# Optimization experiments

Measured on AMD Instinct MI355X. Metric: run time of the kernel, lower is better.

The kernel has to match this reference:

```python
import jax, jax.numpy as jnp
import numpy as np

B, D_IN, D_OUT, N_SUBNET, G = 16384, 512, 512, 8, 2


def setup_inputs() -> dict:
    key = jax.random.key(0)
    k_x, k_g, k_w = jax.random.split(key, 3)
    x = jax.random.normal(k_x, (B, D_IN), dtype=jnp.float32)
    groups = jax.random.randint(k_g, (B, G), 0, N_SUBNET, dtype=jnp.int32)
    # per-expert Dense params (the 'subnets')
    W = jax.random.normal(k_w, (N_SUBNET, D_IN, D_OUT), dtype=jnp.float32) * (1.0 / np.sqrt(D_IN))
    b = jnp.zeros((N_SUBNET, D_OUT), dtype=jnp.float32)
    return {"x": x, "groups": groups, "W": W, "b": b}


def reference(x, groups, W, b):
    """SubnetGate: one-hot gated dispatch to per-group subnets + combine.

    Faithful math: gates = one_hot(groups[:, group_col], n_subnet);
    out = sum_e gates[:, e] * subnet_e(x). Since gates are one-hot the
    combine selects exactly one expert output per row (gate weight 1.0).
    """
    group_col = 0
    n_subnet = W.shape[0]
    idx_group = groups[:, group_col]                     # [B]
    gates = jax.nn.one_hot(idx_group, n_subnet, dtype=x.dtype)  # [B, E]
    # run every expert on the full batch (dense reference for the
    # gather-compute-scatter kernel), then gate-combine
    expert_out = jnp.einsum("bi,eio->beo", x, W) + b[None, :, :]  # [B, E, O]
    out = jnp.einsum("be,beo->bo", gates, expert_out)             # [B, O]
    return out
```

## Files before the change

### kernel.cpp

```cpp
#include <hip/hip_runtime.h>
#include <hip/hip_bf16.h>


#define NROWS   16384
#define KDIM    512
#define NDIM    512
#define NEXP    8
#define BM      64
#define BN      128
#define BK      64
#define NT_PER  4
#define KT_PER  8
#define TILE_ELEMS (BN * BK)
#define WS_ROWLIST_OFF 4096
#define WS_WT_OFF      (4096 + NEXP * NROWS * 4)

typedef __bf16        bf16x8 __attribute__((ext_vector_type(8)));
typedef float         f32x4  __attribute__((ext_vector_type(4)));
typedef unsigned int  u32x4  __attribute__((ext_vector_type(4)));

__device__ __forceinline__ unsigned int f2bf_u(float f) {
    unsigned int u = __builtin_bit_cast(unsigned int, f);
    return (u + 0x7FFFu + ((u >> 16) & 1u)) >> 16;
}

__device__ __forceinline__ void gl_lds16(const void* g, void* l) {
    __builtin_amdgcn_global_load_lds(
        (const __attribute__((address_space(1))) unsigned int*)g,
        (__attribute__((address_space(3))) unsigned int*)l, 16, 0, 0);
}

__device__ __forceinline__ bf16x8 pack_bf8(f32x4 lo, f32x4 hi) {
    u32x4 w;
    w.x = f2bf_u(lo.x) | (f2bf_u(lo.y) << 16);
    w.y = f2bf_u(lo.z) | (f2bf_u(lo.w) << 16);
    w.z = f2bf_u(hi.x) | (f2bf_u(hi.y) << 16);
    w.w = f2bf_u(hi.z) | (f2bf_u(hi.w) << 16);
    return __builtin_bit_cast(bf16x8, w);
}

__global__ void prep_kernel(const float* __restrict__ W,
                            const int* __restrict__ groups,
                            int* __restrict__ gcnt,
                            int* __restrict__ rowlist,
                            unsigned short* __restrict__ Wtile) {
    __shared__ __align__(16) unsigned short tl4[32 * 64];
    __shared__ int lcnt[NEXP];
    __shared__ int lbase[NEXP];
    const int bid = blockIdx.x;
    const int tid = threadIdx.x;

    if (bid < 1024) {
        const int tile = bid >> 2;
        const int qq   = bid & 3;
        const int e  = tile >> 5;
        const int nt = (tile >> 3) & 3;
        const int kt = tile & 7;
        const float* Wb = W + (size_t)e * (KDIM * NDIM);

        const int n   = qq * 32 + (tid & 31);
        const int g   = tid >> 5;
        const int col = nt * BN + n;
        unsigned int p[4];
        #pragma unroll
        for (int jj = 0; jj < 4; ++jj) {
            int k0 = kt * BK + g * 8 + jj * 2;
            unsigned int lo = f2bf_u(Wb[(size_t)k0 * NDIM + col]);
            unsigned int hi = f2bf_u(Wb[(size_t)(k0 + 1) * NDIM + col]);
            p[jj] = lo | (hi << 16);
        }
        *(u32x4*)&tl4[(n & 31) * 64 + (g ^ (n & 7)) * 8] = *(const u32x4*)p;
        __syncthreads();
        unsigned short* dst = Wtile + (size_t)tile * TILE_ELEMS
                                    + ((size_t)qq * 256 + tid) * 8;
        *(u32x4*)dst = *(const u32x4*)&tl4[tid * 8];
    } else {
        const int base = (bid - 1024) * 256;
        if (tid < NEXP) lcnt[tid] = 0;
        __syncthreads();
        int r = base + tid;
        int e = groups[r * 2] & 7;
        int pos = atomicAdd(&lcnt[e], 1);
        __syncthreads();
        if (tid < NEXP) lbase[tid] = atomicAdd(&gcnt[tid], lcnt[tid]);
        __syncthreads();
        rowlist[e * NROWS + lbase[e] + pos] = r;
    }
}

__global__ __launch_bounds__(256, 4)
void gemm_kernel(const float* __restrict__ x,
                 const int* __restrict__ counts,
                 const int* __restrict__ rowlist,
                 const unsigned short* __restrict__ Wtile,
                 const float* __restrict__ bias,
                 float* __restrict__ out) {
    __shared__ __align__(16) unsigned short Bsm[2][TILE_ELEMS];

    const int bid = blockIdx.x;
    const int e   = bid & 7;
    const int j   = bid >> 3;
    const int nt  = j & 3;
    const int mt  = j >> 2;
    const int cnt = counts[e];
    const int rb  = mt * BM;
    if (rb >= cnt) return;
    int m_valid = cnt - rb;
    if (m_valid > BM) m_valid = BM;
    const int* rl = rowlist + e * NROWS + rb;

    const int tid = threadIdx.x;
    const int w   = tid >> 6;
    const int ln  = tid & 63;
    const int q   = ln >> 4;
    const int l15 = ln & 15;

    const int am = w * 16 + l15;
    const float* aptr = x + (size_t)rl[(am < m_valid) ? am : 0] * KDIM + q * 8;

    const unsigned short* wt =
        Wtile + (size_t)((e * NT_PER + nt) * KT_PER) * TILE_ELEMS;

    f32x4 a0, a1, a2, a3;
    f32x4 acc[8];
    #pragma unroll
    for (int ni = 0; ni < 8; ++ni) acc[ni] = (f32x4){0.f, 0.f, 0.f, 0.f};

    #pragma unroll
    for (int i = 0; i < 4; ++i) {
        int off = (i * 256 + tid) * 8;
        gl_lds16(wt + off, &Bsm[0][off]);
    }
    a0 = *(const f32x4*)aptr;
    a1 = *(const f32x4*)(aptr + 4);
    a2 = *(const f32x4*)(aptr + 32);
    a3 = *(const f32x4*)(aptr + 36);

    for (int kt = 0; kt < KT_PER; ++kt) {
        __syncthreads();
        if (kt < KT_PER - 1) {
            const unsigned short* src = wt + (size_t)(kt + 1) * TILE_ELEMS;
            unsigned short* dstl = Bsm[(kt + 1) & 1];
            #pragma unroll
            for (int i = 0; i < 4; ++i) {
                int off = (i * 256 + tid) * 8;
                gl_lds16(src + off, dstl + off);
            }
        }
        bf16x8 af0 = pack_bf8(a0, a1);
        bf16x8 af1 = pack_bf8(a2, a3);
        if (kt < KT_PER - 1) {
            const float* s = aptr + (kt + 1) * BK;
            a0 = *(const f32x4*)s;
            a1 = *(const f32x4*)(s + 4);
            a2 = *(const f32x4*)(s + 32);
            a3 = *(const f32x4*)(s + 36);
        }
        const unsigned short* bcur = Bsm[kt & 1];
        #pragma unroll
        for (int ni = 0; ni < 8; ++ni) {
            int n = ni * 16 + l15;
            bf16x8 b0 = *(const bf16x8*)&bcur[n * 64 + (q ^ (n & 7)) * 8];
            acc[ni] = __builtin_amdgcn_mfma_f32_16x16x32_bf16(af0, b0, acc[ni], 0, 0, 0);
        }
        #pragma unroll
        for (int ni = 0; ni < 8; ++ni) {
            int n = ni * 16 + l15;
            bf16x8 b1 = *(const bf16x8*)&bcur[n * 64 + ((4 + q) ^ (n & 7)) * 8];
            acc[ni] = __builtin_amdgcn_mfma_f32_16x16x32_bf16(af1, b1, acc[ni], 0, 0, 0);
        }
    }

    int grow[4];
    #pragma unroll
    for (int r = 0; r < 4; ++r) {
        int mloc = w * 16 + q * 4 + r;
        grow[r] = (mloc < m_valid) ? rl[mloc] : -1;
    }
    const int ncol0 = nt * BN;
    #pragma unroll
    for (int ni = 0; ni < 8; ++ni) {
        int col = ncol0 + ni * 16 + l15;
        float bv = bias[e * NDIM + col];
        #pragma unroll
        for (int r = 0; r < 4; ++r)
            if (grow[r] >= 0)
                __builtin_nontemporal_store(acc[ni][r] + bv,
                                            &out[(size_t)grow[r] * NDIM + col]);
    }
}

extern "C" void kernel_launch(void* const* d_in, const int* in_sizes, int n_in,
                              void* d_out, int out_size, void* d_ws, size_t ws_size,
                              hipStream_t stream) {
    const float* x      = (const float*)d_in[0];
    const int*   groups = (const int*)d_in[1];
    const float* W      = (const float*)d_in[2];
    const float* b      = (const float*)d_in[3];
    float*       out    = (float*)d_out;

    char* ws = (char*)d_ws;
    int*            counts  = (int*)ws;
    int*            rowlist = (int*)(ws + WS_ROWLIST_OFF);
    unsigned short* Wtile   = (unsigned short*)(ws + WS_WT_OFF);

    hipMemsetAsync(counts, 0, NEXP * sizeof(int), stream);
    prep_kernel<<<1088, 256, 0, stream>>>(W, groups, counts, rowlist, Wtile);
    gemm_kernel<<<8192, 256, 0, stream>>>(x, counts, rowlist, Wtile, b, out);
}
```

Baseline: 128.2 us.

## Double M tile, pre-convert x to bf16, 4-stage B pipeline, ballot-based rowlist

The GEMM M tile grows from 64 to 128 rows, so each wave computes two 16-row fragments and each B tile loaded into LDS is reused twice as much. The prep kernel now also converts x to bf16 in workspace when there is room, halving A-load bytes and removing per-k-step packing in the GEMM. B staging moves to a 4-buffer pipeline with explicit waitcnt, barriers and setprio. Rowlist construction switches from global atomics to a deterministic ballot/prefix scheme with one block per expert, and the memset is dropped. In exchange there is higher register and LDS use (launch bounds 2), an extra pass over x, and a serial 8-block rowlist step.

```diff
diff --git a/kernel.cpp b/kernel.cpp
--- a/kernel.cpp
+++ b/kernel.cpp
@@ -6,7 +6,7 @@
 #define KDIM    512
 #define NDIM    512
 #define NEXP    8
-#define BM      64
+#define BM      128
 #define BN      128
 #define BK      64
 #define NT_PER  4
@@ -14,6 +14,8 @@
 #define TILE_ELEMS (BN * BK)
 #define WS_ROWLIST_OFF 4096
 #define WS_WT_OFF      (4096 + NEXP * NROWS * 4)
+#define WS_XG_OFF      (WS_WT_OFF + (size_t)NEXP * NT_PER * KT_PER * TILE_ELEMS * 2)
+#define WS_NEEDED      (WS_XG_OFF + (size_t)NROWS * KDIM * 2)
 
 typedef __bf16        bf16x8 __attribute__((ext_vector_type(8)));
 typedef float         f32x4  __attribute__((ext_vector_type(4)));
@@ -40,19 +42,58 @@
 }
 
 __global__ void prep_kernel(const float* __restrict__ W,
+                            const float* __restrict__ x,
                             const int* __restrict__ groups,
-                            int* __restrict__ gcnt,
+                            int* __restrict__ counts,
                             int* __restrict__ rowlist,
-                            unsigned short* __restrict__ Wtile) {
-    __shared__ __align__(16) unsigned short tl4[32 * 64];
-    __shared__ int lcnt[NEXP];
-    __shared__ int lbase[NEXP];
+                            unsigned short* __restrict__ Wtile,
+                            unsigned short* __restrict__ xg) {
     const int bid = blockIdx.x;
     const int tid = threadIdx.x;
 
-    if (bid < 1024) {
-        const int tile = bid >> 2;
-        const int qq   = bid & 3;
+    if (bid < 8) {
+        __shared__ int wcnt_s[4];
+        __shared__ int woff_s[4];
+        __shared__ int runb;
+        const int e  = bid;
+        const int w  = tid >> 6;
+        const int ln = tid & 63;
+        const unsigned long long below = (ln == 63) ? ~0ull >> 1
+                                                    : (1ull << ln) - 1;
+        int* dst = rowlist + e * NROWS;
+        if (tid == 0) runb = 0;
+        __syncthreads();
+        for (int it = 0; it < NROWS / 1024; ++it) {
+            int rbase = it * 1024 + tid * 4;
+            u32x4 ga = *(const u32x4*)&groups[rbase * 2];
+            u32x4 gb = *(const u32x4*)&groups[rbase * 2 + 4];
+            bool h0 = ((int)ga.x == e), h1 = ((int)ga.z == e);
+            bool h2 = ((int)gb.x == e), h3 = ((int)gb.z == e);
+            unsigned long long m0 = __ballot(h0), m1 = __ballot(h1);
+            unsigned long long m2 = __ballot(h2), m3 = __ballot(h3);
+            int c0 = __popcll(m0), c1 = __popcll(m1), c2 = __popcll(m2);
+            if (ln == 0) wcnt_s[w] = c0 + c1 + c2 + __popcll(m3);
+            __syncthreads();
+            if (tid == 0) {
+                int s = runb;
+                #pragma unroll
+                for (int i = 0; i < 4; ++i) { woff_s[i] = s; s += wcnt_s[i]; }
+                runb = s;
+            }
+            __syncthreads();
+            int base = woff_s[w];
+            if (h0) dst[base + __popcll(m0 & below)] = rbase;
+            if (h1) dst[base + c0 + __popcll(m1 & below)] = rbase + 1;
+            if (h2) dst[base + c0 + c1 + __popcll(m2 & below)] = rbase + 2;
+            if (h3) dst[base + c0 + c1 + c2 + __popcll(m3 & below)] = rbase + 3;
+            __syncthreads();
+        }
+        if (tid == 0) counts[e] = runb;
+    } else if (bid < 1032) {
+        __shared__ __align__(16) unsigned short tl4[32 * 64];
+        const int tb   = bid - 8;
+        const int tile = tb >> 2;
+        const int qq   = tb & 3;
         const int e  = tile >> 5;
         const int nt = (tile >> 3) & 3;
         const int kt = tile & 7;
@@ -75,27 +116,87 @@
                                     + ((size_t)qq * 256 + tid) * 8;
         *(u32x4*)dst = *(const u32x4*)&tl4[tid * 8];
     } else {
-        const int base = (bid - 1024) * 256;
-        if (tid < NEXP) lcnt[tid] = 0;
-        __syncthreads();
-        int r = base + tid;
-        int e = groups[r * 2] & 7;
-        int pos = atomicAdd(&lcnt[e], 1);
-        __syncthreads();
-        if (tid < NEXP) lbase[tid] = atomicAdd(&gcnt[tid], lcnt[tid]);
-        __syncthreads();
-        rowlist[e * NROWS + lbase[e] + pos] = r;
-    }
-}
-
-__global__ __launch_bounds__(256, 4)
+        const size_t base = ((size_t)(bid - 1032) * 256 + tid) * 16;
+        f32x4 v0 = *(const f32x4*)&x[base];
+        f32x4 v1 = *(const f32x4*)&x[base + 4];
+        f32x4 v2 = *(const f32x4*)&x[base + 8];
+        f32x4 v3 = *(const f32x4*)&x[base + 12];
+        *(bf16x8*)&xg[base]     = pack_bf8(v0, v1);
+        *(bf16x8*)&xg[base + 8] = pack_bf8(v2, v3);
+    }
+}
+
+
+#define STAGE_B(KT, BUF)                                                     \
+    {                                                                        \
+        const unsigned short* _src = wt + (size_t)(KT) * TILE_ELEMS;         \
+        _Pragma("unroll")                                                    \
+        for (int _i = 0; _i < 4; ++_i) {                                     \
+            int _off = (_i * 256 + tid) * 8;                                 \
+            gl_lds16(_src + _off, &Bsm[BUF][_off]);                          \
+        }                                                                    \
+    }
+
+#define LOAD_A_XG(KT, AR)                                                    \
+    {                                                                        \
+        const unsigned short* _p0 = arow0 + (KT) * BK + q * 8;               \
+        const unsigned short* _p1 = arow1 + (KT) * BK + q * 8;               \
+        AR[0][0] = *(const bf16x8*)_p0;                                      \
+        AR[0][1] = *(const bf16x8*)(_p0 + 32);                               \
+        AR[1][0] = *(const bf16x8*)_p1;                                      \
+        AR[1][1] = *(const bf16x8*)(_p1 + 32);                               \
+    }
+
+#define LOAD_A_F32(KT, AR)                                                   \
+    {                                                                        \
+        const float* _p0 = afrow0 + (KT) * BK + q * 8;                       \
+        const float* _p1 = afrow1 + (KT) * BK + q * 8;                       \
+        AR[0][0] = pack_bf8(*(const f32x4*)_p0, *(const f32x4*)(_p0 + 4));   \
+        AR[0][1] = pack_bf8(*(const f32x4*)(_p0 + 32),                       \
+                            *(const f32x4*)(_p0 + 36));                      \
+        AR[1][0] = pack_bf8(*(const f32x4*)_p1, *(const f32x4*)(_p1 + 4));   \
+        AR[1][1] = pack_bf8(*(const f32x4*)(_p1 + 32),                       \
+                            *(const f32x4*)(_p1 + 36));                      \
+    }
+
+#define COMPUTE(BUF, AR)                                                     \
+    {                                                                        \
+        _Pragma("unroll")                                                    \
+        for (int _h = 0; _h < 2; ++_h) {                                     \
+            _Pragma("unroll")                                                \
+            for (int _ni = 0; _ni < 8; ++_ni) {                              \
+                int _n = _ni * 16 + l15;                                     \
+                bf16x8 _bf = *(const bf16x8*)&Bsm[BUF][_n * 64 +             \
+                             ((_h * 4 + q) ^ (_n & 7)) * 8];                 \
+                acc[0][_ni] = __builtin_amdgcn_mfma_f32_16x16x32_bf16(       \
+                    AR[0][_h], _bf, acc[0][_ni], 0, 0, 0);                   \
+                acc[1][_ni] = __builtin_amdgcn_mfma_f32_16x16x32_bf16(       \
+                    AR[1][_h], _bf, acc[1][_ni], 0, 0, 0);                   \
+            }                                                                \
+        }                                                                    \
+    }
+
+#define KSTEP(KT, ACUR, ANXT, LOADA)                                         \
+    {                                                                        \
+        asm volatile("s_waitcnt vmcnt(12)" ::: "memory");                    \
+        __builtin_amdgcn_s_barrier();                                        \
+        __builtin_amdgcn_sched_barrier(0);                                   \
+        if ((KT) + 3 < KT_PER) STAGE_B((KT) + 3, ((KT) + 3) & 3)             \
+        if ((KT) + 1 < KT_PER) LOADA((KT) + 1, ANXT)                         \
+        __builtin_amdgcn_s_setprio(1);                                       \
+        COMPUTE((KT) & 3, ACUR)                                              \
+        __builtin_amdgcn_s_setprio(0);                                       \
+    }
+
+__global__ __launch_bounds__(256, 2)
 void gemm_kernel(const float* __restrict__ x,
+                 const unsigned short* __restrict__ xg,
                  const int* __restrict__ counts,
                  const int* __restrict__ rowlist,
                  const unsigned short* __restrict__ Wtile,
                  const float* __restrict__ bias,
                  float* __restrict__ out) {
-    __shared__ __align__(16) unsigned short Bsm[2][TILE_ELEMS];
+    __shared__ __align__(16) unsigned short Bsm[4][TILE_ELEMS];
 
     const int bid = blockIdx.x;
     const int e   = bid & 7;
@@ -114,79 +215,75 @@
     const int ln  = tid & 63;
     const int q   = ln >> 4;
     const int l15 = ln & 15;
-
-    const int am = w * 16 + l15;
-    const float* aptr = x + (size_t)rl[(am < m_valid) ? am : 0] * KDIM + q * 8;
+    const int wm  = w * 32;
+
+    const int r0i = wm + l15;
+    const int r1i = wm + 16 + l15;
+    const int ri0 = (r0i < m_valid) ? r0i : 0;
+    const int ri1 = (r1i < m_valid) ? r1i : 0;
 
     const unsigned short* wt =
         Wtile + (size_t)((e * NT_PER + nt) * KT_PER) * TILE_ELEMS;
 
-    f32x4 a0, a1, a2, a3;
-    f32x4 acc[8];
+    f32x4 acc[2][8];
     #pragma unroll
-    for (int ni = 0; ni < 8; ++ni) acc[ni] = (f32x4){0.f, 0.f, 0.f, 0.f};
-
+    for (int mi = 0; mi < 2; ++mi)
+        #pragma unroll
+        for (int ni = 0; ni < 8; ++ni)
+            acc[mi][ni] = (f32x4){0.f, 0.f, 0.f, 0.f};
+
+    bf16x8 aA[2][2], aB[2][2];
+
+    STAGE_B(0, 0)
+    STAGE_B(1, 1)
+    STAGE_B(2, 2)
+
+    if (xg != nullptr) {
+        const unsigned short* arow0 = xg + (size_t)rl[ri0] * KDIM;
+        const unsigned short* arow1 = xg + (size_t)rl[ri1] * KDIM;
+        LOAD_A_XG(0, aA)
+        KSTEP(0, aA, aB, LOAD_A_XG)
+        KSTEP(1, aB, aA, LOAD_A_XG)
+        KSTEP(2, aA, aB, LOAD_A_XG)
+        KSTEP(3, aB, aA, LOAD_A_XG)
+        KSTEP(4, aA, aB, LOAD_A_XG)
+        KSTEP(5, aB, aA, LOAD_A_XG)
+        KSTEP(6, aA, aB, LOAD_A_XG)
+        KSTEP(7, aB, aA, LOAD_A_XG)
+    } else {
+        const float* afrow0 = x + (size_t)rl[ri0] * KDIM;
+        const float* afrow1 = x + (size_t)rl[ri1] * KDIM;
+        LOAD_A_F32(0, aA)
+        KSTEP(0, aA, aB, LOAD_A_F32)
+        KSTEP(1, aB, aA, LOAD_A_F32)
+        KSTEP(2, aA, aB, LOAD_A_F32)
+        KSTEP(3, aB, aA, LOAD_A_F32)
+        KSTEP(4, aA, aB, LOAD_A_F32)
+        KSTEP(5, aB, aA, LOAD_A_F32)
+        KSTEP(6, aA, aB, LOAD_A_F32)
+        KSTEP(7, aB, aA, LOAD_A_F32)
+    }
+
+    int grow[2][4];
     #pragma unroll
-    for (int i = 0; i < 4; ++i) {
-        int off = (i * 256 + tid) * 8;
-        gl_lds16(wt + off, &Bsm[0][off]);
-    }
-    a0 = *(const f32x4*)aptr;
-    a1 = *(const f32x4*)(aptr + 4);
-    a2 = *(const f32x4*)(aptr + 32);
-    a3 = *(const f32x4*)(aptr + 36);
-
-    for (int kt = 0; kt < KT_PER; ++kt) {
-        __syncthreads();
-        if (kt < KT_PER - 1) {
-            const unsigned short* src = wt + (size_t)(kt + 1) * TILE_ELEMS;
-            unsigned short* dstl = Bsm[(kt + 1) & 1];
-            #pragma unroll
-            for (int i = 0; i < 4; ++i) {
-                int off = (i * 256 + tid) * 8;
-                gl_lds16(src + off, dstl + off);
-            }
+    for (int mi = 0; mi < 2; ++mi)
+        #pragma unroll
+        for (int r = 0; r < 4; ++r) {
+            int mloc = wm + mi * 16 + q * 4 + r;
+            grow[mi][r] = (mloc < m_valid) ? rl[mloc] : -1;
         }
-        bf16x8 af0 = pack_bf8(a0, a1);
-        bf16x8 af1 = pack_bf8(a2, a3);
-        if (kt < KT_PER - 1) {
-            const float* s = aptr + (kt + 1) * BK;
-            a0 = *(const f32x4*)s;
-            a1 = *(const f32x4*)(s + 4);
-            a2 = *(const f32x4*)(s + 32);
-            a3 = *(const f32x4*)(s + 36);
-        }
-        const unsigned short* bcur = Bsm[kt & 1];
-        #pragma unroll
-        for (int ni = 0; ni < 8; ++ni) {
-            int n = ni * 16 + l15;
-            bf16x8 b0 = *(const bf16x8*)&bcur[n * 64 + (q ^ (n & 7)) * 8];
-            acc[ni] = __builtin_amdgcn_mfma_f32_16x16x32_bf16(af0, b0, acc[ni], 0, 0, 0);
-        }
-        #pragma unroll
-        for (int ni = 0; ni < 8; ++ni) {
-            int n = ni * 16 + l15;
-            bf16x8 b1 = *(const bf16x8*)&bcur[n * 64 + ((4 + q) ^ (n & 7)) * 8];
-            acc[ni] = __builtin_amdgcn_mfma_f32_16x16x32_bf16(af1, b1, acc[ni], 0, 0, 0);
-        }
-    }
-
-    int grow[4];
-    #pragma unroll
-    for (int r = 0; r < 4; ++r) {
-        int mloc = w * 16 + q * 4 + r;
-        grow[r] = (mloc < m_valid) ? rl[mloc] : -1;
-    }
     const int ncol0 = nt * BN;
     #pragma unroll
     for (int ni = 0; ni < 8; ++ni) {
         int col = ncol0 + ni * 16 + l15;
         float bv = bias[e * NDIM + col];
         #pragma unroll
-        for (int r = 0; r < 4; ++r)
-            if (grow[r] >= 0)
-                __builtin_nontemporal_store(acc[ni][r] + bv,
-                                            &out[(size_t)grow[r] * NDIM + col]);
+        for (int mi = 0; mi < 2; ++mi)
+            #pragma unroll
+            for (int r = 0; r < 4; ++r)
+                if (grow[mi][r] >= 0)
+                    __builtin_nontemporal_store(acc[mi][ni][r] + bv,
+                        &out[(size_t)grow[mi][r] * NDIM + col]);
     }
 }
 
@@ -203,8 +300,10 @@
     int*            counts  = (int*)ws;
     int*            rowlist = (int*)(ws + WS_ROWLIST_OFF);
     unsigned short* Wtile   = (unsigned short*)(ws + WS_WT_OFF);
-
-    hipMemsetAsync(counts, 0, NEXP * sizeof(int), stream);
-    prep_kernel<<<1088, 256, 0, stream>>>(W, groups, counts, rowlist, Wtile);
-    gemm_kernel<<<8192, 256, 0, stream>>>(x, counts, rowlist, Wtile, b, out);
-}
+    const bool use_xg = (ws_size >= WS_NEEDED);
+    unsigned short* xg = use_xg ? (unsigned short*)(ws + WS_XG_OFF) : nullptr;
+
+    prep_kernel<<<use_xg ? 3080 : 1032, 256, 0, stream>>>(
+        W, x, groups, counts, rowlist, Wtile, xg);
+    gemm_kernel<<<4096, 256, 0, stream>>>(x, xg, counts, rowlist, Wtile, b, out);
+}
```

New measurement: 132.4 us. 1.03x slower.
